# Kernel tuning notes

Hardware: AMD Instinct MI355X
Metric: run time of the kernel (lower is better)

Reference implementation:

```python
import jax, jax.numpy as jnp
import numpy as np
import math

B, L, D, H = 4, 1024, 512, 8
TAU = 0.1
LN_EPS = 1e-5


def _attn(xq, xk, xv, wq, bq, wk, bk, wv, bv, wo, bo, energy=None, threshold=None):
    Bq, Lq, Dm = xq.shape
    Dh = Dm // H
    Q = (xq @ wq.T + bq).reshape(Bq, Lq, H, Dh)
    K = (xk @ wk.T + bk).reshape(Bq, -1, H, Dh)
    V = (xv @ wv.T + bv).reshape(Bq, -1, H, Dh)
    sc = jnp.einsum('bqhd,bkhd->bhqk', Q, K) / jnp.sqrt(jnp.float32(Dh))
    if energy is not None:
        # mask keys whose mean |energy| over channels is below threshold
        mask = jnp.abs(energy).mean(-1)[:, None, None, :] > threshold  # (B,1,1,Lk)
        sc = jnp.where(mask, sc, -jnp.inf)
    w = jnp.nan_to_num(jax.nn.softmax(sc, axis=-1))  # nan->0 for fully-masked rows
    o = jnp.einsum('bhqk,bkhd->bqhd', w, V).reshape(Bq, Lq, Dm)
    return o @ wo.T + bo


def _ln(x, w, b):
    m = x.mean(-1, keepdims=True)
    v = x.var(-1, keepdims=True)
    return (x - m) / jnp.sqrt(v + LN_EPS) * w + b


def _mlp(x, w1, b1, w2, b2):
    h = jax.nn.gelu(x @ w1.T + b1, approximate=False)  # torch nn.GELU default = exact
    return h @ w2.T + b2


def setup_inputs():
    key = jax.random.key(0)
    ks = list(jax.random.split(key, 64))

    def nxt():
        return ks.pop(0)

    def w(shape, scale=0.02):
        return jax.random.normal(nxt(), shape, dtype=jnp.float32) * scale

    inp = {
        'LL': jax.random.normal(nxt(), (B, D, L), dtype=jnp.float32),
        'LH': jax.random.normal(nxt(), (B, D, L), dtype=jnp.float32),
        'raw_tau': jnp.float32(math.log(TAU / (1.0 - TAU))),
    }
    for p in ('llA', 'lhA', 'crA'):
        for nm in ('q', 'k', 'v', 'o'):
            inp[f'{p}_w{nm}'] = w((D, D))
            inp[f'{p}_b{nm}'] = jnp.zeros((D,), jnp.float32)
    for p in ('mlp_ll', 'mlp_lh'):
        inp[f'{p}_w1'] = w((4 * D, D))
        inp[f'{p}_b1'] = jnp.zeros((4 * D,), jnp.float32)
        inp[f'{p}_w2'] = w((D, 4 * D))
        inp[f'{p}_b2'] = jnp.zeros((D,), jnp.float32)
    inp['n1_w'] = jnp.ones((D,), jnp.float32)
    inp['n1_b'] = jnp.zeros((D,), jnp.float32)
    inp['n2_w'] = jnp.ones((D,), jnp.float32)
    inp['n2_b'] = jnp.zeros((D,), jnp.float32)
    return inp


def reference(LL, LH, raw_tau,
              llA_wq, llA_bq, llA_wk, llA_bk, llA_wv, llA_bv, llA_wo, llA_bo,
              lhA_wq, lhA_bq, lhA_wk, lhA_bk, lhA_wv, lhA_bv, lhA_wo, lhA_bo,
              crA_wq, crA_bq, crA_wk, crA_bk, crA_wv, crA_bv, crA_wo, crA_bo,
              mlp_ll_w1, mlp_ll_b1, mlp_ll_w2, mlp_ll_b2,
              mlp_lh_w1, mlp_lh_b1, mlp_lh_w2, mlp_lh_b2,
              n1_w, n1_b, n2_w, n2_b):
    tau = jax.nn.sigmoid(raw_tau)
    ll_s = jnp.transpose(LL, (0, 2, 1))  # (B,L,D)
    lh_s = jnp.transpose(LH, (0, 2, 1))
    ll_o = _attn(ll_s, ll_s, ll_s, llA_wq, llA_bq, llA_wk, llA_bk, llA_wv, llA_bv, llA_wo, llA_bo)
    lh_o = _attn(lh_s, lh_s, lh_s, lhA_wq, lhA_bq, lhA_wk, lhA_bk, lhA_wv, lhA_bv, lhA_wo, lhA_bo,
                 energy=lh_s, threshold=tau)
    cr_o = _attn(ll_o, lh_o, lh_o, crA_wq, crA_bq, crA_wk, crA_bk, crA_wv, crA_bv, crA_wo, crA_bo)
    ll_f = _ln(ll_s + ll_o + cr_o, n1_w, n1_b)
    ll_f = _mlp(ll_f, mlp_ll_w1, mlp_ll_b1, mlp_ll_w2, mlp_ll_b2) + ll_f
    lh_f = _ln(lh_s + lh_o, n2_w, n2_b)
    lh_f = _mlp(lh_f, mlp_lh_w1, mlp_lh_b1, mlp_lh_w2, mlp_lh_b2) + lh_f
    return (jnp.transpose(ll_f, (0, 2, 1)), jnp.transpose(lh_f, (0, 2, 1)))
```

## Files before the change

kernel.cpp:

```cpp
#include <hip/hip_runtime.h>
#include <hip/hip_bf16.h>
#include <stdint.h>

typedef unsigned short u16;
typedef __bf16 bf16_t;
typedef bf16_t bf16x8 __attribute__((ext_vector_type(8)));
typedef float f32x4 __attribute__((ext_vector_type(4)));

#define DEV static __device__ __forceinline__

DEV u16 f2b(float f) {
    __hip_bfloat16 h = __float2bfloat16(f);
    return __builtin_bit_cast(u16, h);
}

DEV bf16x8 ld_frag(const u16* p) {
    uint4 u = *reinterpret_cast<const uint4*>(p);
    return __builtin_bit_cast(bf16x8, u);
}

DEV float gelu(float v) {
    float y = 0.79788456080286536f * (v + 0.044715f * v * v * v);
    float e = __expf(-2.f * fabsf(y));
    float th = (1.f - e) / (1.f + e);
    th = copysignf(th, y);
    return 0.5f * v * (1.f + th);
}

DEV void gl_lds16(const u16* g, u16* l) {
    __builtin_amdgcn_global_load_lds(
        (const __attribute__((address_space(1))) void*)(uintptr_t)g,
        (__attribute__((address_space(3))) void*)(unsigned int)(uintptr_t)l,
        16, 0, 0);
}

struct ConvEnt { const float* s; u16* d; int n; };
struct ConvArgs { ConvEnt e[16]; };

__global__ __launch_bounds__(256) void k_conv(ConvArgs a) {
    const ConvEnt en = a.e[blockIdx.y];
    for (int i = (blockIdx.x * 256 + threadIdx.x) * 4; i < en.n; i += 256 * 256 * 4) {
        const float4 f = *reinterpret_cast<const float4*>(en.s + i);
        unsigned r0 = (unsigned)f2b(f.x) | ((unsigned)f2b(f.y) << 16);
        unsigned r1 = (unsigned)f2b(f.z) | ((unsigned)f2b(f.w) << 16);
        uint2 rr; rr.x = r0; rr.y = r1;
        *reinterpret_cast<uint2*>(en.d + i) = rr;
    }
}

struct CpyEnt { const float* s; float* d; };
struct CpyArgs { CpyEnt e[8]; };

__global__ __launch_bounds__(256) void k_cpyf(CpyArgs a) {
    const CpyEnt en = a.e[blockIdx.y];
    int i = blockIdx.x * 256 + threadIdx.x;
    en.d[i] = en.s[i];
}

__global__ __launch_bounds__(256) void k_tin(const float* __restrict__ LL, const float* __restrict__ LH,
                                             float* __restrict__ llf, u16* __restrict__ llb,
                                             float* __restrict__ lhf, u16* __restrict__ lhb) {
    __shared__ float t[32][33];
    int z = blockIdx.z, b = z & 3;
    const float* in = (z < 4) ? LL : LH;
    float* of = (z < 4) ? llf : lhf;
    u16* ob = (z < 4) ? llb : lhb;
    int l0 = blockIdx.x * 32, d0 = blockIdx.y * 32;
    int tx = threadIdx.x, ty = threadIdx.y;
#pragma unroll
    for (int j = 0; j < 4; ++j) {
        int d = d0 + ty + j * 8;
        t[ty + j * 8][tx] = in[((size_t)b * 512 + d) * 1024 + l0 + tx];
    }
    __syncthreads();
#pragma unroll
    for (int j = 0; j < 4; ++j) {
        int l = l0 + ty + j * 8;
        float v = t[tx][ty + j * 8];
        size_t o = ((size_t)b * 1024 + l) * 512 + d0 + tx;
        of[o] = v;
        ob[o] = f2b(v);
    }
}

__global__ __launch_bounds__(256) void k_tout(const float* __restrict__ y0, const float* __restrict__ y1,
                                              float* __restrict__ out) {
    __shared__ float t[32][33];
    int z = blockIdx.z, b = z & 3;
    const float* in = (z < 4) ? y0 : y1;
    float* o = out + ((z < 4) ? 0 : (size_t)4096 * 512);
    int l0 = blockIdx.x * 32, d0 = blockIdx.y * 32;
    int tx = threadIdx.x, ty = threadIdx.y;
#pragma unroll
    for (int j = 0; j < 4; ++j) {
        int l = l0 + ty + j * 8;
        t[ty + j * 8][tx] = in[((size_t)b * 1024 + l) * 512 + d0 + tx];
    }
    __syncthreads();
#pragma unroll
    for (int j = 0; j < 4; ++j) {
        int d = d0 + ty + j * 8;
        o[((size_t)b * 512 + d) * 1024 + l0 + tx] = t[tx][ty + j * 8];
    }
}

__global__ __launch_bounds__(256) void k_mask(const float* __restrict__ lh_s,
                                              const float* __restrict__ raw_tau,
                                              float* __restrict__ kbias) {
    int row = blockIdx.x * 4 + (threadIdx.x >> 6);
    int lane = threadIdx.x & 63;
    const float* p = lh_s + (size_t)row * 512 + lane * 8;
    float s = 0.f;
#pragma unroll
    for (int j = 0; j < 8; ++j) s += fabsf(p[j]);
#pragma unroll
    for (int m = 32; m >= 1; m >>= 1) s += __shfl_xor(s, m, 64);
    float tau = 1.f / (1.f + expf(-raw_tau[0]));
    if (lane == 0) kbias[row] = (s * (1.f / 512.f) > tau) ? 0.f : -3.0e38f;
}

__global__ __launch_bounds__(256) void k_ln(const float* __restrict__ a, const float* __restrict__ b,
                                            const float* __restrict__ c, const float* __restrict__ w,
                                            const float* __restrict__ bi,
                                            float* __restrict__ of, u16* __restrict__ ob) {
    int row = blockIdx.x * 4 + (threadIdx.x >> 6);
    int lane = threadIdx.x & 63;
    size_t base = (size_t)row * 512 + lane * 8;
    float x[8];
#pragma unroll
    for (int j = 0; j < 8; ++j) {
        float v = a[base + j] + b[base + j];
        if (c) v += c[base + j];
        x[j] = v;
    }
    float s = 0.f, s2 = 0.f;
#pragma unroll
    for (int j = 0; j < 8; ++j) { s += x[j]; s2 += x[j] * x[j]; }
#pragma unroll
    for (int m = 32; m >= 1; m >>= 1) { s += __shfl_xor(s, m, 64); s2 += __shfl_xor(s2, m, 64); }
    float mean = s * (1.f / 512.f);
    float var = s2 * (1.f / 512.f) - mean * mean;
    float rs = rsqrtf(var + 1e-5f);
#pragma unroll
    for (int j = 0; j < 8; ++j) {
        float y = (x[j] - mean) * rs * w[lane * 8 + j] + bi[lane * 8 + j];
        of[base + j] = y;
        ob[base + j] = f2b(y);
    }
}

struct GP {
    const u16* A; const u16* W; const float* bias; const float* res;
    float* Cf; u16* Cb; u16* Qp; u16* Kp; u16* Vt;
    int N, K, kB, vB, nwg;
};

template <int BM, int BN, int GELU_ACT, int PACK>
__global__ __launch_bounds__(256) void k_gemm(GP p0, GP p1, int M) {
    constexpr int BK = 64;
    __shared__ alignas(16) u16 Al[2][BM * BK];
    __shared__ alignas(16) u16 Wl[2][BN * BK];
    GP g = (blockIdx.y == 0) ? p0 : p1;
    const int orig = blockIdx.x;
    if (orig >= g.nwg) return;
    int bid;
    {
        const int xcd = orig & 7, lin = orig >> 3;
        const int q = g.nwg >> 3, r = g.nwg & 7;
        bid = (xcd < r ? xcd * (q + 1) : r * (q + 1) + (xcd - r) * q) + lin;
    }
    const int K = g.K, N = g.N;
    const int nny = N / BN;
    const int m0 = (bid / nny) * BM, n0 = (bid % nny) * BN;

    const int t = threadIdx.x, w = t >> 6, l = t & 63;
    constexpr int FM = BM / 32, FN = BN / 32;
    const int wr = w >> 1, wc = w & 1;
    const int lq = l & 15, lg = l >> 4;
    f32x4 acc[FM][FN] = {};

    const int srow = l >> 3, schunk = l & 7;
    auto stage = [&](int kcol, int buf) {
#pragma unroll
        for (int i = 0; i < BM / 32; ++i) {
            const int row = i * 32 + w * 8 + srow;
            gl_lds16(g.A + (size_t)(m0 + row) * K + kcol + ((schunk ^ (row & 7)) * 8),
                     &Al[buf][(i * 32 + w * 8) * BK]);
        }
#pragma unroll
        for (int i = 0; i < BN / 32; ++i) {
            const int row = i * 32 + w * 8 + srow;
            gl_lds16(g.W + (size_t)(n0 + row) * K + kcol + ((schunk ^ (row & 7)) * 8),
                     &Wl[buf][(i * 32 + w * 8) * BK]);
        }
    };

    stage(0, 0);
    const int KT = K / BK;
    for (int kt = 0; kt < KT; ++kt) {
        const int cur = kt & 1;
        __syncthreads();
        if (kt + 1 < KT) stage((kt + 1) * BK, cur ^ 1);
#pragma unroll
        for (int s = 0; s < 2; ++s) {
            bf16x8 af[FM], bw[FN];
#pragma unroll
            for (int i = 0; i < FM; ++i) {
                const int row = wr * (BM / 2) + i * 16 + lq;
                af[i] = ld_frag(&Al[cur][row * BK + (((s * 4 + lg) ^ (row & 7)) * 8)]);
            }
#pragma unroll
            for (int j = 0; j < FN; ++j) {
                const int row = wc * (BN / 2) + j * 16 + lq;
                bw[j] = ld_frag(&Wl[cur][row * BK + (((s * 4 + lg) ^ (row & 7)) * 8)]);
            }
#pragma unroll
            for (int i = 0; i < FM; ++i)
#pragma unroll
                for (int j = 0; j < FN; ++j)
                    acc[i][j] = __builtin_amdgcn_mfma_f32_16x16x32_bf16(af[i], bw[j], acc[i][j], 0, 0, 0);
        }
    }

    if (PACK && n0 >= g.vB) {
        u16* T = (u16*)Al;
        constexpr int CH = BM / 8, CMASK = CH - 1, SH = (CH == 16) ? 4 : 3;
        __syncthreads();
#pragma unroll
        for (int i = 0; i < FM; ++i) {
#pragma unroll
            for (int j = 0; j < FN; ++j) {
                const int ni = wc * (BN / 2) + j * 16 + lq;
                const float bn = g.bias[n0 + ni];
#pragma unroll
                for (int r2 = 0; r2 < 4; ++r2) {
                    const int mi = wr * (BM / 2) + i * 16 + lg * 4 + r2;
                    T[ni * BM + (((mi >> 3) ^ (ni & CMASK)) * 8) + (mi & 7)] = f2b(acc[i][j][r2] + bn);
                }
            }
        }
        __syncthreads();
        const int bb = m0 >> 10, mloc = m0 & 1023;
        const int mc = t & CMASK, nib = t >> SH;
        constexpr int RPP = 256 / CH;
#pragma unroll
        for (int p2 = 0; p2 < BN / RPP; ++p2) {
            const int ni = nib + p2 * RPP;
            uint4 u = *reinterpret_cast<const uint4*>(&T[ni * BM + ((mc ^ (ni & CMASK)) * 8)]);
            const int d = n0 - g.vB + ni;
            *reinterpret_cast<uint4*>(
                &g.Vt[((size_t)(bb * 8 + (d >> 6)) * 64 + (d & 63)) * 1024 + mloc + mc * 8]) = u;
        }
        return;
    }

#pragma unroll
    for (int i = 0; i < FM; ++i) {
#pragma unroll
        for (int j = 0; j < FN; ++j) {
            const int n = n0 + wc * (BN / 2) + j * 16 + lq;
            const float bn = g.bias[n];
#pragma unroll
            for (int r2 = 0; r2 < 4; ++r2) {
                const int m = m0 + wr * (BM / 2) + i * 16 + lg * 4 + r2;
                float v = acc[i][j][r2] + bn;
                if (GELU_ACT) v = gelu(v);
                if (PACK) {
                    const int bb = m >> 10, ll_ = m & 1023;
                    if (n >= g.kB) {
                        const int d = n - g.kB;
                        g.Kp[((size_t)(bb * 8 + (d >> 6)) * 1024 + ll_) * 64 + (d & 63)] = f2b(v);
                    } else {
                        g.Qp[((size_t)(bb * 8 + (n >> 6)) * 1024 + ll_) * 64 + (n & 63)] = f2b(v * 0.125f);
                    }
                } else {
                    size_t o = (size_t)m * N + n;
                    if (g.res) v += g.res[o];
                    if (g.Cf) g.Cf[o] = v;
                    if (g.Cb) g.Cb[o] = f2b(v);
                }
            }
        }
    }
}

__global__ __launch_bounds__(256) void k_attn(const u16* __restrict__ Qp, const u16* __restrict__ Kp,
                                              const u16* __restrict__ Vtp, u16* __restrict__ O,
                                              const float* __restrict__ kbias, int nwg) {
    constexpr int L = 1024;
    __shared__ alignas(16) u16 Kl[2][64 * 64];
    __shared__ alignas(16) u16 Vl[2][64 * 64];
    __shared__ alignas(16) u16 Pl[128 * 64];
    const int t = threadIdx.x, w = t >> 6, l = t & 63;
    const int bid = ((int)blockIdx.x & 7) * (nwg >> 3) + ((int)blockIdx.x >> 3);
    const int bh = bid >> 3, q0 = (bid & 7) * 128;
    const int bz = bh >> 3, h = bh & 7;
    const int lq = l & 15, lg = l >> 4;
    const float* kb = (kbias != nullptr && bz >= 4) ? (kbias + (size_t)(bz - 4) * L) : nullptr;

    bf16x8 qa[2][2];
#pragma unroll
    for (int i = 0; i < 2; ++i) {
        const u16* qp = Qp + ((size_t)bh * L + q0 + w * 32 + i * 16 + lq) * 64 + lg * 8;
        qa[i][0] = ld_frag(qp);
        qa[i][1] = ld_frag(qp + 32);
    }

    const int r0 = w * 16 + (l >> 3), r1 = r0 + 8, c = l & 7;
    const u16* Ksrc0 = Kp + (size_t)bh * L * 64 + (size_t)r0 * 64 + ((c ^ (r0 & 7)) * 8);
    const u16* Ksrc1 = Kp + (size_t)bh * L * 64 + (size_t)r1 * 64 + ((c ^ (r1 & 7)) * 8);
    const u16* Vsrc0 = Vtp + (size_t)bh * 64 * L + (size_t)r0 * L + ((c ^ (r0 & 7)) * 8);
    const u16* Vsrc1 = Vtp + (size_t)bh * 64 * L + (size_t)r1 * L + ((c ^ (r1 & 7)) * 8);

    auto stage = [&](int k0, int buf) {
        gl_lds16(Ksrc0 + (size_t)k0 * 64, &Kl[buf][(w * 16) * 64]);
        gl_lds16(Ksrc1 + (size_t)k0 * 64, &Kl[buf][(w * 16 + 8) * 64]);
        gl_lds16(Vsrc0 + k0, &Vl[buf][(w * 16) * 64]);
        gl_lds16(Vsrc1 + k0, &Vl[buf][(w * 16 + 8) * 64]);
    };

    int addrA[4][2];
#pragma unroll
    for (int f = 0; f < 4; ++f) {
        int row = f * 16 + lq;
#pragma unroll
        for (int s = 0; s < 2; ++s) addrA[f][s] = row * 64 + (((s * 4 + lg) ^ (row & 7)) * 8);
    }
    int paddr[2][2], pwbase[2];
#pragma unroll
    for (int i = 0; i < 2; ++i) {
        const int prow = w * 32 + i * 16 + lq;
#pragma unroll
        for (int s = 0; s < 2; ++s) paddr[i][s] = prow * 64 + (((s * 4 + lg) ^ (prow & 7)) * 8);
        pwbase[i] = w * 32 + i * 16 + lg * 4;
    }

    f32x4 oacc[2][4] = {};
    float lrow[2][4] = {};

    stage(0, 0);
    for (int kt = 0; kt < 16; ++kt) {
        const int cur = kt & 1;
        __syncthreads();
        if (kt + 1 < 16) stage((kt + 1) * 64, cur ^ 1);

        f32x4 sc[2][4];
#pragma unroll
        for (int f = 0; f < 4; ++f) {
            bf16x8 k0 = ld_frag(&Kl[cur][addrA[f][0]]);
            bf16x8 k1 = ld_frag(&Kl[cur][addrA[f][1]]);
#pragma unroll
            for (int i = 0; i < 2; ++i) {
                f32x4 a = {};
                a = __builtin_amdgcn_mfma_f32_16x16x32_bf16(qa[i][0], k0, a, 0, 0, 0);
                a = __builtin_amdgcn_mfma_f32_16x16x32_bf16(qa[i][1], k1, a, 0, 0, 0);
                sc[i][f] = a;
            }
        }
#pragma unroll
        for (int f = 0; f < 4; ++f) {
            float bv = kb ? kb[kt * 64 + f * 16 + lq] : 0.f;
#pragma unroll
            for (int i = 0; i < 2; ++i) {
#pragma unroll
                for (int r = 0; r < 4; ++r) {
                    float pv = __expf(sc[i][f][r] + bv);
                    lrow[i][r] += pv;
                    const int prow = pwbase[i] + r;
                    Pl[prow * 64 + (((f * 2 + (lq >> 3)) ^ (prow & 7)) * 8) + (lq & 7)] = f2b(pv);
                }
            }
        }
        bf16x8 pa[2][2];
#pragma unroll
        for (int i = 0; i < 2; ++i) {
            pa[i][0] = ld_frag(&Pl[paddr[i][0]]);
            pa[i][1] = ld_frag(&Pl[paddr[i][1]]);
        }
#pragma unroll
        for (int db = 0; db < 4; ++db) {
            bf16x8 v0 = ld_frag(&Vl[cur][addrA[db][0]]);
            bf16x8 v1 = ld_frag(&Vl[cur][addrA[db][1]]);
#pragma unroll
            for (int i = 0; i < 2; ++i) {
                oacc[i][db] = __builtin_amdgcn_mfma_f32_16x16x32_bf16(pa[i][0], v0, oacc[i][db], 0, 0, 0);
                oacc[i][db] = __builtin_amdgcn_mfma_f32_16x16x32_bf16(pa[i][1], v1, oacc[i][db], 0, 0, 0);
            }
        }
    }
#pragma unroll
    for (int i = 0; i < 2; ++i)
#pragma unroll
        for (int r = 0; r < 4; ++r) {
            float v = lrow[i][r];
#pragma unroll
            for (int msk = 8; msk >= 1; msk >>= 1) v += __shfl_xor(v, msk, 16);
            lrow[i][r] = v;
        }
#pragma unroll
    for (int i = 0; i < 2; ++i) {
#pragma unroll
        for (int db = 0; db < 4; ++db) {
#pragma unroll
            for (int r = 0; r < 4; ++r) {
                float denom = lrow[i][r];
                float v = (denom > 0.f) ? oacc[i][db][r] / denom : 0.f;
                O[((size_t)bz * L + q0 + w * 32 + i * 16 + lg * 4 + r) * 512 + h * 64 + db * 16 + lq] = f2b(v);
            }
        }
    }
}

extern "C" void kernel_launch(void* const* d_in, const int* in_sizes, int n_in,
                              void* d_out, int out_size, void* d_ws, size_t ws_size,
                              hipStream_t stream) {
    const int M = 4096;
    const float* LL = (const float*)d_in[0];
    const float* LH = (const float*)d_in[1];
    const float* raw_tau = (const float*)d_in[2];
    auto F = [&](int i) { return (const float*)d_in[i]; };
    const int BIG = 1 << 28;

    char* p = (char*)d_ws;
    auto alloc = [&](size_t bytes) { void* r = (void*)p; p += (bytes + 255) & ~(size_t)255; return r; };
    const size_t MDf = (size_t)M * 512 * 4, MDb = (size_t)M * 512 * 2;
    float* ll_s_f = (float*)alloc(MDf);
    float* lh_s_f = (float*)alloc(MDf);
    u16* ll_s_b = (u16*)alloc(MDb);
    u16* lh_s_b = (u16*)alloc(MDb);
    u16* Qp = (u16*)alloc(2 * MDb);
    u16* Kp = (u16*)alloc(2 * MDb);
    u16* Vt = (u16*)alloc(2 * MDb);
    u16* Cxb = (u16*)alloc(2 * MDb);
    float* ll_o_f = (float*)alloc(MDf);
    u16* ll_o_b = (u16*)alloc(MDb);
    float* lh_o_f = (float*)alloc(MDf);
    u16* lh_o_b = (u16*)alloc(MDb);
    float* cr_o_f = (float*)alloc(MDf);
    float* ln_f_ll = (float*)alloc(MDf);
    float* ln_f_lh = (float*)alloc(MDf);
    u16* ln_b = (u16*)alloc(MDb);
    u16* hb = (u16*)alloc((size_t)M * 2048 * 2);
    float* yf_ll = (float*)alloc(MDf);
    float* yf_lh = (float*)alloc(MDf);
    float* kbias = (float*)alloc(4096 * 4);
    float* bqkv_ll = (float*)alloc(1536 * 4);
    float* bqkv_lh = (float*)alloc(1536 * 4);
    float* bkv_cr = (float*)alloc(1024 * 4);
    const size_t WDD = (size_t)262144;
    u16* wqkv_ll = (u16*)alloc(3 * WDD * 2);
    u16* wqkv_lh = (u16*)alloc(3 * WDD * 2);
    u16* wkv_cr = (u16*)alloc(2 * WDD * 2);
    u16* wq_cr = (u16*)alloc(WDD * 2);
    u16* wo_ll = (u16*)alloc(WDD * 2);
    u16* wo_lh = (u16*)alloc(WDD * 2);
    u16* wo_cr = (u16*)alloc(WDD * 2);
    u16* wm[4];
    for (int i = 0; i < 4; ++i) wm[i] = (u16*)alloc((size_t)1048576 * 2);

    const size_t SET = (size_t)4 * 8 * 1024 * 64;

    ConvArgs ca;
    ca.e[0] = {F(3), wqkv_ll, (int)WDD};
    ca.e[1] = {F(5), wqkv_ll + WDD, (int)WDD};
    ca.e[2] = {F(7), wqkv_ll + 2 * WDD, (int)WDD};
    ca.e[3] = {F(11), wqkv_lh, (int)WDD};
    ca.e[4] = {F(13), wqkv_lh + WDD, (int)WDD};
    ca.e[5] = {F(15), wqkv_lh + 2 * WDD, (int)WDD};
    ca.e[6] = {F(19), wq_cr, (int)WDD};
    ca.e[7] = {F(21), wkv_cr, (int)WDD};
    ca.e[8] = {F(23), wkv_cr + WDD, (int)WDD};
    ca.e[9] = {F(9), wo_ll, (int)WDD};
    ca.e[10] = {F(17), wo_lh, (int)WDD};
    ca.e[11] = {F(25), wo_cr, (int)WDD};
    ca.e[12] = {F(27), wm[0], 1048576};
    ca.e[13] = {F(29), wm[1], 1048576};
    ca.e[14] = {F(31), wm[2], 1048576};
    ca.e[15] = {F(33), wm[3], 1048576};
    k_conv<<<dim3(256, 16), 256, 0, stream>>>(ca);

    CpyArgs cp;
    cp.e[0] = {F(4), bqkv_ll};
    cp.e[1] = {F(6), bqkv_ll + 512};
    cp.e[2] = {F(8), bqkv_ll + 1024};
    cp.e[3] = {F(12), bqkv_lh};
    cp.e[4] = {F(14), bqkv_lh + 512};
    cp.e[5] = {F(16), bqkv_lh + 1024};
    cp.e[6] = {F(22), bkv_cr};
    cp.e[7] = {F(24), bkv_cr + 512};
    k_cpyf<<<dim3(2, 8), 256, 0, stream>>>(cp);

    k_tin<<<dim3(32, 16, 8), dim3(32, 8), 0, stream>>>(LL, LH, ll_s_f, ll_s_b, lh_s_f, lh_s_b);
    k_mask<<<dim3(1024), 256, 0, stream>>>(lh_s_f, raw_tau, kbias);

    auto gp = [&](const u16* A, const u16* W, const float* bias, int N, int K, int nwg) {
        GP g = {};
        g.A = A; g.W = W; g.bias = bias; g.N = N; g.K = K; g.nwg = nwg;
        g.kB = BIG; g.vB = BIG;
        return g;
    };

    {
        GP a = gp(ll_s_b, wqkv_ll, bqkv_ll, 1536, 512, 384);
        a.kB = 512; a.vB = 1024; a.Qp = Qp; a.Kp = Kp; a.Vt = Vt;
        GP b = gp(lh_s_b, wqkv_lh, bqkv_lh, 1536, 512, 384);
        b.kB = 512; b.vB = 1024; b.Qp = Qp + SET; b.Kp = Kp + SET; b.Vt = Vt + SET;
        k_gemm<128, 128, 0, 1><<<dim3(384, 2), 256, 0, stream>>>(a, b, M);
    }
    k_attn<<<dim3(512), 256, 0, stream>>>(Qp, Kp, Vt, Cxb, kbias, 512);
    {
        GP a = gp(Cxb, wo_ll, F(10), 512, 512, 512);
        a.Cf = ll_o_f; a.Cb = ll_o_b;
        GP b = gp(Cxb + SET, wo_lh, F(18), 512, 512, 512);
        b.Cf = lh_o_f; b.Cb = lh_o_b;
        k_gemm<64, 64, 0, 0><<<dim3(512, 2), 256, 0, stream>>>(a, b, M);
    }
    k_ln<<<dim3(1024), 256, 0, stream>>>(lh_s_f, lh_o_f, nullptr, F(37), F(38), ln_f_lh, ln_b);
    {
        GP a = gp(ln_b, wm[2], F(32), 2048, 512, 512);
        a.Cb = hb;
        k_gemm<128, 128, 1, 0><<<dim3(512, 1), 256, 0, stream>>>(a, a, M);
    }
    {
        GP a = gp(ll_o_b, wq_cr, F(20), 512, 512, 512);
        a.Qp = Qp;
        GP b = gp(lh_o_b, wkv_cr, bkv_cr, 1024, 512, 1024);
        b.kB = 0; b.vB = 512; b.Kp = Kp; b.Vt = Vt;
        k_gemm<64, 64, 0, 1><<<dim3(1024, 2), 256, 0, stream>>>(a, b, M);
    }
    k_attn<<<dim3(256), 256, 0, stream>>>(Qp, Kp, Vt, Cxb, nullptr, 256);
    {
        GP a = gp(Cxb, wo_cr, F(26), 512, 512, 512);
        a.Cf = cr_o_f;
        GP b = gp(hb, wm[3], F(34), 512, 2048, 512);
        b.Cf = yf_lh; b.res = ln_f_lh;
        k_gemm<64, 64, 0, 0><<<dim3(512, 2), 256, 0, stream>>>(a, b, M);
    }
    k_ln<<<dim3(1024), 256, 0, stream>>>(ll_s_f, ll_o_f, cr_o_f, F(35), F(36), ln_f_ll, ln_b);
    {
        GP a = gp(ln_b, wm[0], F(28), 2048, 512, 512);
        a.Cb = hb;
        k_gemm<128, 128, 1, 0><<<dim3(512, 1), 256, 0, stream>>>(a, a, M);
    }
    {
        GP a = gp(hb, wm[1], F(30), 512, 2048, 512);
        a.Cf = yf_ll; a.res = ln_f_ll;
        k_gemm<64, 64, 0, 0><<<dim3(512, 1), 256, 0, stream>>>(a, a, M);
    }
    k_tout<<<dim3(32, 16, 8), dim3(32, 8), 0, stream>>>(yf_ll, yf_lh, (float*)d_out);
}
```

Baseline: 268.7 us.

## Fuse attention and independent GEMMs into shared launches to overlap work

Splits the GEMM and attention kernels into device bodies, then adds a combined kernel whose first blocks run attention and whose remaining blocks run an independent GEMM. The LL and LH branches and the cross-attention stages are rescheduled so that attention for one branch overlaps with projection or MLP GEMMs of another, which cuts launch count and fills idle CUs during the low-occupancy attention launches. The Q scale changes to fold in log2(e) so softmax can use exp2f, and the mask bias becomes -inf. This adds shared-memory sizing constraints and load imbalance risk between the mixed block types.

```diff
diff --git a/kernel.cpp b/kernel.cpp
--- a/kernel.cpp
+++ b/kernel.cpp
@@ -8,6 +8,8 @@
 typedef float f32x4 __attribute__((ext_vector_type(4)));
 
 #define DEV static __device__ __forceinline__
+
+#define QSCALE 0.18033688011112042f
 
 DEV u16 f2b(float f) {
     __hip_bfloat16 h = __float2bfloat16(f);
@@ -116,7 +118,7 @@
 #pragma unroll
     for (int m = 32; m >= 1; m >>= 1) s += __shfl_xor(s, m, 64);
     float tau = 1.f / (1.f + expf(-raw_tau[0]));
-    if (lane == 0) kbias[row] = (s * (1.f / 512.f) > tau) ? 0.f : -3.0e38f;
+    if (lane == 0) kbias[row] = (s * (1.f / 512.f) > tau) ? 0.f : -__builtin_inff();
 }
 
 __global__ __launch_bounds__(256) void k_ln(const float* __restrict__ a, const float* __restrict__ b,
@@ -152,17 +154,14 @@
 struct GP {
     const u16* A; const u16* W; const float* bias; const float* res;
     float* Cf; u16* Cb; u16* Qp; u16* Kp; u16* Vt;
-    int N, K, kB, vB, nwg;
+    int N, K, kB, vB, nwg, pack;
 };
 
 template <int BM, int BN, int GELU_ACT, int PACK>
-__global__ __launch_bounds__(256) void k_gemm(GP p0, GP p1, int M) {
+DEV void gemm_body(u16* smem, const GP g, int orig, int M) {
     constexpr int BK = 64;
-    __shared__ alignas(16) u16 Al[2][BM * BK];
-    __shared__ alignas(16) u16 Wl[2][BN * BK];
-    GP g = (blockIdx.y == 0) ? p0 : p1;
-    const int orig = blockIdx.x;
-    if (orig >= g.nwg) return;
+    u16* Al = smem;
+    u16* Wl = smem + 2 * BM * BK;
     int bid;
     {
         const int xcd = orig & 7, lin = orig >> 3;
@@ -185,13 +184,13 @@
         for (int i = 0; i < BM / 32; ++i) {
             const int row = i * 32 + w * 8 + srow;
             gl_lds16(g.A + (size_t)(m0 + row) * K + kcol + ((schunk ^ (row & 7)) * 8),
-                     &Al[buf][(i * 32 + w * 8) * BK]);
+                     &Al[buf * BM * BK + (i * 32 + w * 8) * BK]);
         }
 #pragma unroll
         for (int i = 0; i < BN / 32; ++i) {
             const int row = i * 32 + w * 8 + srow;
             gl_lds16(g.W + (size_t)(n0 + row) * K + kcol + ((schunk ^ (row & 7)) * 8),
-                     &Wl[buf][(i * 32 + w * 8) * BK]);
+                     &Wl[buf * BN * BK + (i * 32 + w * 8) * BK]);
         }
     };
 
@@ -207,12 +206,12 @@
 #pragma unroll
             for (int i = 0; i < FM; ++i) {
                 const int row = wr * (BM / 2) + i * 16 + lq;
-                af[i] = ld_frag(&Al[cur][row * BK + (((s * 4 + lg) ^ (row & 7)) * 8)]);
+                af[i] = ld_frag(&Al[cur * BM * BK + row * BK + (((s * 4 + lg) ^ (row & 7)) * 8)]);
             }
 #pragma unroll
             for (int j = 0; j < FN; ++j) {
                 const int row = wc * (BN / 2) + j * 16 + lq;
-                bw[j] = ld_frag(&Wl[cur][row * BK + (((s * 4 + lg) ^ (row & 7)) * 8)]);
+                bw[j] = ld_frag(&Wl[cur * BN * BK + row * BK + (((s * 4 + lg) ^ (row & 7)) * 8)]);
             }
 #pragma unroll
             for (int i = 0; i < FM; ++i)
@@ -222,8 +221,8 @@
         }
     }
 
-    if (PACK && n0 >= g.vB) {
-        u16* T = (u16*)Al;
+    if (PACK && g.pack && n0 >= g.vB) {
+        u16* T = Al;
         constexpr int CH = BM / 8, CMASK = CH - 1, SH = (CH == 16) ? 4 : 3;
         __syncthreads();
 #pragma unroll
@@ -265,13 +264,13 @@
                 const int m = m0 + wr * (BM / 2) + i * 16 + lg * 4 + r2;
                 float v = acc[i][j][r2] + bn;
                 if (GELU_ACT) v = gelu(v);
-                if (PACK) {
+                if (PACK && g.pack) {
                     const int bb = m >> 10, ll_ = m & 1023;
                     if (n >= g.kB) {
                         const int d = n - g.kB;
                         g.Kp[((size_t)(bb * 8 + (d >> 6)) * 1024 + ll_) * 64 + (d & 63)] = f2b(v);
                     } else {
-                        g.Qp[((size_t)(bb * 8 + (n >> 6)) * 1024 + ll_) * 64 + (n & 63)] = f2b(v * 0.125f);
+                        g.Qp[((size_t)(bb * 8 + (n >> 6)) * 1024 + ll_) * 64 + (n & 63)] = f2b(v * QSCALE);
                     }
                 } else {
                     size_t o = (size_t)m * N + n;
@@ -284,39 +283,47 @@
     }
 }
 
-__global__ __launch_bounds__(256) void k_attn(const u16* __restrict__ Qp, const u16* __restrict__ Kp,
-                                              const u16* __restrict__ Vtp, u16* __restrict__ O,
-                                              const float* __restrict__ kbias, int nwg) {
+template <int BM, int BN, int GELU_ACT, int PACK>
+__global__ __launch_bounds__(256) void k_gemm(GP p0, GP p1, int M) {
+    __shared__ alignas(16) u16 smem[2 * (BM + BN) * 64];
+    GP g = (blockIdx.y == 0) ? p0 : p1;
+    if ((int)blockIdx.x >= g.nwg) return;
+    gemm_body<BM, BN, GELU_ACT, PACK>(smem, g, blockIdx.x, M);
+}
+
+struct AT { const u16* Qp; const u16* Kp; const u16* Vt; u16* O; const float* kbias; };
+
+DEV void attn_body(u16* smem, const AT a, int orig, int nwg) {
     constexpr int L = 1024;
-    __shared__ alignas(16) u16 Kl[2][64 * 64];
-    __shared__ alignas(16) u16 Vl[2][64 * 64];
-    __shared__ alignas(16) u16 Pl[128 * 64];
+    u16* Pl = smem + 16384;
     const int t = threadIdx.x, w = t >> 6, l = t & 63;
-    const int bid = ((int)blockIdx.x & 7) * (nwg >> 3) + ((int)blockIdx.x >> 3);
+    const int bid = (orig & 7) * (nwg >> 3) + (orig >> 3);
     const int bh = bid >> 3, q0 = (bid & 7) * 128;
     const int bz = bh >> 3, h = bh & 7;
     const int lq = l & 15, lg = l >> 4;
-    const float* kb = (kbias != nullptr && bz >= 4) ? (kbias + (size_t)(bz - 4) * L) : nullptr;
+    const float* kb = a.kbias ? (a.kbias + (size_t)bz * L) : nullptr;
 
     bf16x8 qa[2][2];
 #pragma unroll
     for (int i = 0; i < 2; ++i) {
-        const u16* qp = Qp + ((size_t)bh * L + q0 + w * 32 + i * 16 + lq) * 64 + lg * 8;
+        const u16* qp = a.Qp + ((size_t)bh * L + q0 + w * 32 + i * 16 + lq) * 64 + lg * 8;
         qa[i][0] = ld_frag(qp);
         qa[i][1] = ld_frag(qp + 32);
     }
 
     const int r0 = w * 16 + (l >> 3), r1 = r0 + 8, c = l & 7;
-    const u16* Ksrc0 = Kp + (size_t)bh * L * 64 + (size_t)r0 * 64 + ((c ^ (r0 & 7)) * 8);
-    const u16* Ksrc1 = Kp + (size_t)bh * L * 64 + (size_t)r1 * 64 + ((c ^ (r1 & 7)) * 8);
-    const u16* Vsrc0 = Vtp + (size_t)bh * 64 * L + (size_t)r0 * L + ((c ^ (r0 & 7)) * 8);
-    const u16* Vsrc1 = Vtp + (size_t)bh * 64 * L + (size_t)r1 * L + ((c ^ (r1 & 7)) * 8);
+    const u16* Ksrc0 = a.Kp + (size_t)bh * L * 64 + (size_t)r0 * 64 + ((c ^ (r0 & 7)) * 8);
+    const u16* Ksrc1 = a.Kp + (size_t)bh * L * 64 + (size_t)r1 * 64 + ((c ^ (r1 & 7)) * 8);
+    const u16* Vsrc0 = a.Vt + (size_t)bh * 64 * L + (size_t)r0 * L + ((c ^ (r0 & 7)) * 8);
+    const u16* Vsrc1 = a.Vt + (size_t)bh * 64 * L + (size_t)r1 * L + ((c ^ (r1 & 7)) * 8);
 
     auto stage = [&](int k0, int buf) {
-        gl_lds16(Ksrc0 + (size_t)k0 * 64, &Kl[buf][(w * 16) * 64]);
-        gl_lds16(Ksrc1 + (size_t)k0 * 64, &Kl[buf][(w * 16 + 8) * 64]);
-        gl_lds16(Vsrc0 + k0, &Vl[buf][(w * 16) * 64]);
-        gl_lds16(Vsrc1 + k0, &Vl[buf][(w * 16 + 8) * 64]);
+        u16* Kb = smem + buf * 4096;
+        u16* Vb = smem + 8192 + buf * 4096;
+        gl_lds16(Ksrc0 + (size_t)k0 * 64, &Kb[(w * 16) * 64]);
+        gl_lds16(Ksrc1 + (size_t)k0 * 64, &Kb[(w * 16 + 8) * 64]);
+        gl_lds16(Vsrc0 + k0, &Vb[(w * 16) * 64]);
+        gl_lds16(Vsrc1 + k0, &Vb[(w * 16 + 8) * 64]);
     };
 
     int addrA[4][2];
@@ -341,20 +348,22 @@
     stage(0, 0);
     for (int kt = 0; kt < 16; ++kt) {
         const int cur = kt & 1;
+        u16* Kc = smem + cur * 4096;
+        u16* Vc = smem + 8192 + cur * 4096;
         __syncthreads();
         if (kt + 1 < 16) stage((kt + 1) * 64, cur ^ 1);
 
         f32x4 sc[2][4];
 #pragma unroll
         for (int f = 0; f < 4; ++f) {
-            bf16x8 k0 = ld_frag(&Kl[cur][addrA[f][0]]);
-            bf16x8 k1 = ld_frag(&Kl[cur][addrA[f][1]]);
+            bf16x8 k0 = ld_frag(&Kc[addrA[f][0]]);
+            bf16x8 k1 = ld_frag(&Kc[addrA[f][1]]);
 #pragma unroll
             for (int i = 0; i < 2; ++i) {
-                f32x4 a = {};
-                a = __builtin_amdgcn_mfma_f32_16x16x32_bf16(qa[i][0], k0, a, 0, 0, 0);
-                a = __builtin_amdgcn_mfma_f32_16x16x32_bf16(qa[i][1], k1, a, 0, 0, 0);
-                sc[i][f] = a;
+                f32x4 acc = {};
+                acc = __builtin_amdgcn_mfma_f32_16x16x32_bf16(qa[i][0], k0, acc, 0, 0, 0);
+                acc = __builtin_amdgcn_mfma_f32_16x16x32_bf16(qa[i][1], k1, acc, 0, 0, 0);
+                sc[i][f] = acc;
             }
         }
 #pragma unroll
@@ -364,7 +373,7 @@
             for (int i = 0; i < 2; ++i) {
 #pragma unroll
                 for (int r = 0; r < 4; ++r) {
-                    float pv = __expf(sc[i][f][r] + bv);
+                    float pv = exp2f(sc[i][f][r] + bv);
                     lrow[i][r] += pv;
                     const int prow = pwbase[i] + r;
                     Pl[prow * 64 + (((f * 2 + (lq >> 3)) ^ (prow & 7)) * 8) + (lq & 7)] = f2b(pv);
@@ -379,8 +388,8 @@
         }
 #pragma unroll
         for (int db = 0; db < 4; ++db) {
-            bf16x8 v0 = ld_frag(&Vl[cur][addrA[db][0]]);
-            bf16x8 v1 = ld_frag(&Vl[cur][addrA[db][1]]);
+            bf16x8 v0 = ld_frag(&Vc[addrA[db][0]]);
+            bf16x8 v1 = ld_frag(&Vc[addrA[db][1]]);
 #pragma unroll
             for (int i = 0; i < 2; ++i) {
                 oacc[i][db] = __builtin_amdgcn_mfma_f32_16x16x32_bf16(pa[i][0], v0, oacc[i][db], 0, 0, 0);
@@ -405,10 +414,21 @@
             for (int r = 0; r < 4; ++r) {
                 float denom = lrow[i][r];
                 float v = (denom > 0.f) ? oacc[i][db][r] / denom : 0.f;
-                O[((size_t)bz * L + q0 + w * 32 + i * 16 + lg * 4 + r) * 512 + h * 64 + db * 16 + lq] = f2b(v);
-            }
-        }
-    }
+                a.O[((size_t)bz * L + q0 + w * 32 + i * 16 + lg * 4 + r) * 512 + h * 64 + db * 16 + lq] = f2b(v);
+            }
+        }
+    }
+}
+
+template <int BM, int BN, int GELU_ACT, int PACK>
+__global__ __launch_bounds__(256) void k_fattn(AT a, GP g, int nAttn, int M) {
+    constexpr int GS = 2 * (BM + BN) * 64;
+    constexpr int SZ = (GS > 24576) ? GS : 24576;
+    __shared__ alignas(16) u16 smem[SZ];
+    if ((int)blockIdx.x < nAttn)
+        attn_body(smem, a, blockIdx.x, nAttn);
+    else
+        gemm_body<BM, BN, GELU_ACT, PACK>(smem, g, blockIdx.x - nAttn, M);
 }
 
 extern "C" void kernel_launch(void* const* d_in, const int* in_sizes, int n_in,
@@ -496,39 +516,46 @@
     auto gp = [&](const u16* A, const u16* W, const float* bias, int N, int K, int nwg) {
         GP g = {};
         g.A = A; g.W = W; g.bias = bias; g.N = N; g.K = K; g.nwg = nwg;
-        g.kB = BIG; g.vB = BIG;
+        g.kB = BIG; g.vB = BIG; g.pack = 0;
         return g;
     };
 
     {
         GP a = gp(ll_s_b, wqkv_ll, bqkv_ll, 1536, 512, 384);
-        a.kB = 512; a.vB = 1024; a.Qp = Qp; a.Kp = Kp; a.Vt = Vt;
-        GP b = gp(lh_s_b, wqkv_lh, bqkv_lh, 1536, 512, 384);
-        b.kB = 512; b.vB = 1024; b.Qp = Qp + SET; b.Kp = Kp + SET; b.Vt = Vt + SET;
-        k_gemm<128, 128, 0, 1><<<dim3(384, 2), 256, 0, stream>>>(a, b, M);
-    }
-    k_attn<<<dim3(512), 256, 0, stream>>>(Qp, Kp, Vt, Cxb, kbias, 512);
-    {
-        GP a = gp(Cxb, wo_ll, F(10), 512, 512, 512);
-        a.Cf = ll_o_f; a.Cb = ll_o_b;
-        GP b = gp(Cxb + SET, wo_lh, F(18), 512, 512, 512);
-        b.Cf = lh_o_f; b.Cb = lh_o_b;
-        k_gemm<64, 64, 0, 0><<<dim3(512, 2), 256, 0, stream>>>(a, b, M);
+        a.pack = 1; a.kB = 512; a.vB = 1024; a.Qp = Qp; a.Kp = Kp; a.Vt = Vt;
+        k_gemm<128, 128, 0, 1><<<dim3(384, 1), 256, 0, stream>>>(a, a, M);
+    }
+    {
+        AT at = {Qp, Kp, Vt, Cxb, nullptr};
+        GP g = gp(lh_s_b, wqkv_lh, bqkv_lh, 1536, 512, 384);
+        g.pack = 1; g.kB = 512; g.vB = 1024; g.Qp = Qp + SET; g.Kp = Kp + SET; g.Vt = Vt + SET;
+        k_fattn<128, 128, 0, 1><<<dim3(640), 256, 0, stream>>>(at, g, 256, M);
+    }
+    {
+        AT at = {Qp + SET, Kp + SET, Vt + SET, Cxb + SET, kbias};
+        GP g = gp(Cxb, wo_ll, F(10), 512, 512, 512);
+        g.Cf = ll_o_f; g.Cb = ll_o_b;
+        k_fattn<64, 64, 0, 1><<<dim3(768), 256, 0, stream>>>(at, g, 256, M);
+    }
+    {
+        GP a = gp(Cxb + SET, wo_lh, F(18), 512, 512, 512);
+        a.Cf = lh_o_f; a.Cb = lh_o_b;
+        GP b = gp(ll_o_b, wq_cr, F(20), 512, 512, 512);
+        b.pack = 1; b.Qp = Qp;
+        k_gemm<64, 64, 0, 1><<<dim3(512, 2), 256, 0, stream>>>(a, b, M);
     }
     k_ln<<<dim3(1024), 256, 0, stream>>>(lh_s_f, lh_o_f, nullptr, F(37), F(38), ln_f_lh, ln_b);
     {
-        GP a = gp(ln_b, wm[2], F(32), 2048, 512, 512);
-        a.Cb = hb;
-        k_gemm<128, 128, 1, 0><<<dim3(512, 1), 256, 0, stream>>>(a, a, M);
-    }
-    {
-        GP a = gp(ll_o_b, wq_cr, F(20), 512, 512, 512);
-        a.Qp = Qp;
-        GP b = gp(lh_o_b, wkv_cr, bkv_cr, 1024, 512, 1024);
-        b.kB = 0; b.vB = 512; b.Kp = Kp; b.Vt = Vt;
-        k_gemm<64, 64, 0, 1><<<dim3(1024, 2), 256, 0, stream>>>(a, b, M);
-    }
-    k_attn<<<dim3(256), 256, 0, stream>>>(Qp, Kp, Vt, Cxb, nullptr, 256);
+        GP a = gp(lh_o_b, wkv_cr, bkv_cr, 1024, 512, 1024);
+        a.pack = 1; a.kB = 0; a.vB = 512; a.Kp = Kp; a.Vt = Vt;
+        k_gemm<64, 64, 0, 1><<<dim3(1024, 1), 256, 0, stream>>>(a, a, M);
+    }
+    {
+        AT at = {Qp, Kp, Vt, Cxb, nullptr};
+        GP g = gp(ln_b, wm[2], F(32), 2048, 512, 512);
+        g.Cb = hb;
+        k_fattn<128, 128, 1, 0><<<dim3(768), 256, 0, stream>>>(at, g, 256, M);
+    }
     {
         GP a = gp(Cxb, wo_cr, F(26), 512, 512, 512);
         a.Cf = cr_o_f;
```

New measurement: 298.1 us. 10.9% more time.

## Split attention over key halves with separate combine kernel, use exp2 and setprio

Applied to the files above, without the earlier changes.

Attention work is split along the key dimension into two halves per query tile, doubling the number of workgroups. Each half writes unnormalized fp32 numerators and row sums to scratch, and a new combine kernel adds the halves and normalizes. Q is now prescaled by log2(e)/8 so exp2f can replace __expf, the mask bias becomes -inf, and s_setprio is raised around the MFMA sections. This adds a scratch round trip and an extra launch in exchange for higher occupancy. There is no running-max subtraction, so overflow behaviour depends on the score magnitudes.

```diff
diff --git a/kernel.cpp b/kernel.cpp
--- a/kernel.cpp
+++ b/kernel.cpp
@@ -8,6 +8,8 @@
 typedef float f32x4 __attribute__((ext_vector_type(4)));
 
 #define DEV static __device__ __forceinline__
+
+#define QSCALE 0.18033688011112042f
 
 DEV u16 f2b(float f) {
     __hip_bfloat16 h = __float2bfloat16(f);
@@ -116,7 +118,7 @@
 #pragma unroll
     for (int m = 32; m >= 1; m >>= 1) s += __shfl_xor(s, m, 64);
     float tau = 1.f / (1.f + expf(-raw_tau[0]));
-    if (lane == 0) kbias[row] = (s * (1.f / 512.f) > tau) ? 0.f : -3.0e38f;
+    if (lane == 0) kbias[row] = (s * (1.f / 512.f) > tau) ? 0.f : -__builtin_inff();
 }
 
 __global__ __launch_bounds__(256) void k_ln(const float* __restrict__ a, const float* __restrict__ b,
@@ -271,7 +273,7 @@
                         const int d = n - g.kB;
                         g.Kp[((size_t)(bb * 8 + (d >> 6)) * 1024 + ll_) * 64 + (d & 63)] = f2b(v);
                     } else {
-                        g.Qp[((size_t)(bb * 8 + (n >> 6)) * 1024 + ll_) * 64 + (n & 63)] = f2b(v * 0.125f);
+                        g.Qp[((size_t)(bb * 8 + (n >> 6)) * 1024 + ll_) * 64 + (n & 63)] = f2b(v * QSCALE);
                     }
                 } else {
                     size_t o = (size_t)m * N + n;
@@ -284,19 +286,23 @@
     }
 }
 
-__global__ __launch_bounds__(256) void k_attn(const u16* __restrict__ Qp, const u16* __restrict__ Kp,
-                                              const u16* __restrict__ Vtp, u16* __restrict__ O,
-                                              const float* __restrict__ kbias, int nwg) {
+__global__ __launch_bounds__(256) void k_attnK(const u16* __restrict__ Qp, const u16* __restrict__ Kp,
+                                               const u16* __restrict__ Vtp,
+                                               float* __restrict__ numW, float* __restrict__ denW,
+                                               const float* __restrict__ kbias, int nwg) {
     constexpr int L = 1024;
     __shared__ alignas(16) u16 Kl[2][64 * 64];
     __shared__ alignas(16) u16 Vl[2][64 * 64];
     __shared__ alignas(16) u16 Pl[128 * 64];
     const int t = threadIdx.x, w = t >> 6, l = t & 63;
     const int bid = ((int)blockIdx.x & 7) * (nwg >> 3) + ((int)blockIdx.x >> 3);
-    const int bh = bid >> 3, q0 = (bid & 7) * 128;
+    const int item = bid >> 1, half = bid & 1;
+    const int bh = item >> 3, q0 = (item & 7) * 128;
     const int bz = bh >> 3, h = bh & 7;
+    (void)h;
     const int lq = l & 15, lg = l >> 4;
     const float* kb = (kbias != nullptr && bz >= 4) ? (kbias + (size_t)(bz - 4) * L) : nullptr;
+    const int kbase = half * 512;
 
     bf16x8 qa[2][2];
 #pragma unroll
@@ -338,13 +344,14 @@
     f32x4 oacc[2][4] = {};
     float lrow[2][4] = {};
 
-    stage(0, 0);
-    for (int kt = 0; kt < 16; ++kt) {
+    stage(kbase, 0);
+    for (int kt = 0; kt < 8; ++kt) {
         const int cur = kt & 1;
         __syncthreads();
-        if (kt + 1 < 16) stage((kt + 1) * 64, cur ^ 1);
+        if (kt + 1 < 8) stage(kbase + (kt + 1) * 64, cur ^ 1);
 
         f32x4 sc[2][4];
+        __builtin_amdgcn_s_setprio(1);
 #pragma unroll
         for (int f = 0; f < 4; ++f) {
             bf16x8 k0 = ld_frag(&Kl[cur][addrA[f][0]]);
@@ -357,14 +364,15 @@
                 sc[i][f] = a;
             }
         }
+        __builtin_amdgcn_s_setprio(0);
 #pragma unroll
         for (int f = 0; f < 4; ++f) {
-            float bv = kb ? kb[kt * 64 + f * 16 + lq] : 0.f;
+            float bv = kb ? kb[kbase + kt * 64 + f * 16 + lq] : 0.f;
 #pragma unroll
             for (int i = 0; i < 2; ++i) {
 #pragma unroll
                 for (int r = 0; r < 4; ++r) {
-                    float pv = __expf(sc[i][f][r] + bv);
+                    float pv = exp2f(sc[i][f][r] + bv);
                     lrow[i][r] += pv;
                     const int prow = pwbase[i] + r;
                     Pl[prow * 64 + (((f * 2 + (lq >> 3)) ^ (prow & 7)) * 8) + (lq & 7)] = f2b(pv);
@@ -377,6 +385,7 @@
             pa[i][0] = ld_frag(&Pl[paddr[i][0]]);
             pa[i][1] = ld_frag(&Pl[paddr[i][1]]);
         }
+        __builtin_amdgcn_s_setprio(1);
 #pragma unroll
         for (int db = 0; db < 4; ++db) {
             bf16x8 v0 = ld_frag(&Vl[cur][addrA[db][0]]);
@@ -387,6 +396,7 @@
                 oacc[i][db] = __builtin_amdgcn_mfma_f32_16x16x32_bf16(pa[i][1], v1, oacc[i][db], 0, 0, 0);
             }
         }
+        __builtin_amdgcn_s_setprio(0);
     }
 #pragma unroll
     for (int i = 0; i < 2; ++i)
@@ -397,17 +407,49 @@
             for (int msk = 8; msk >= 1; msk >>= 1) v += __shfl_xor(v, msk, 16);
             lrow[i][r] = v;
         }
+    float* nw = numW + (size_t)bid * 8192;
 #pragma unroll
     for (int i = 0; i < 2; ++i) {
 #pragma unroll
         for (int db = 0; db < 4; ++db) {
 #pragma unroll
             for (int r = 0; r < 4; ++r) {
-                float denom = lrow[i][r];
-                float v = (denom > 0.f) ? oacc[i][db][r] / denom : 0.f;
-                O[((size_t)bz * L + q0 + w * 32 + i * 16 + lg * 4 + r) * 512 + h * 64 + db * 16 + lq] = f2b(v);
-            }
-        }
+                nw[(pwbase[i] + r) * 64 + db * 16 + lq] = oacc[i][db][r];
+            }
+        }
+    }
+    if (lq == 0) {
+#pragma unroll
+        for (int i = 0; i < 2; ++i)
+#pragma unroll
+            for (int r = 0; r < 4; ++r) denW[(size_t)bid * 128 + pwbase[i] + r] = lrow[i][r];
+    }
+}
+
+__global__ __launch_bounds__(256) void k_comb(const float* __restrict__ numW,
+                                              const float* __restrict__ denW,
+                                              u16* __restrict__ O) {
+    const int item = blockIdx.x, t = threadIdx.x;
+    const int bh = item >> 3, q0 = (item & 7) * 128;
+    const int bz = bh >> 3, h = bh & 7;
+    const float4* n0 = (const float4*)(numW + (size_t)(item * 2) * 8192);
+    const float4* n1 = (const float4*)(numW + (size_t)(item * 2 + 1) * 8192);
+    const float* d0 = denW + (size_t)(item * 2) * 128;
+    const float* d1 = denW + (size_t)(item * 2 + 1) * 128;
+#pragma unroll
+    for (int e = 0; e < 8; ++e) {
+        const int g = e * 256 + t;
+        const int row = g >> 4, c4 = (g & 15) * 4;
+        float4 a = n0[g], b = n1[g];
+        float den = d0[row] + d1[row];
+        float inv = (den > 0.f) ? 1.f / den : 0.f;
+        u16 o4[4];
+        o4[0] = f2b((a.x + b.x) * inv);
+        o4[1] = f2b((a.y + b.y) * inv);
+        o4[2] = f2b((a.z + b.z) * inv);
+        o4[3] = f2b((a.w + b.w) * inv);
+        *reinterpret_cast<uint2*>(&O[((size_t)bz * 1024 + q0 + row) * 512 + h * 64 + c4]) =
+            *reinterpret_cast<uint2*>(o4);
     }
 }
 
@@ -447,6 +489,8 @@
     float* bqkv_ll = (float*)alloc(1536 * 4);
     float* bqkv_lh = (float*)alloc(1536 * 4);
     float* bkv_cr = (float*)alloc(1024 * 4);
+    float* numW = (float*)alloc((size_t)1024 * 8192 * 4);
+    float* denW = (float*)alloc((size_t)1024 * 128 * 4);
     const size_t WDD = (size_t)262144;
     u16* wqkv_ll = (u16*)alloc(3 * WDD * 2);
     u16* wqkv_lh = (u16*)alloc(3 * WDD * 2);
@@ -507,7 +551,8 @@
         b.kB = 512; b.vB = 1024; b.Qp = Qp + SET; b.Kp = Kp + SET; b.Vt = Vt + SET;
         k_gemm<128, 128, 0, 1><<<dim3(384, 2), 256, 0, stream>>>(a, b, M);
     }
-    k_attn<<<dim3(512), 256, 0, stream>>>(Qp, Kp, Vt, Cxb, kbias, 512);
+    k_attnK<<<dim3(1024), 256, 0, stream>>>(Qp, Kp, Vt, numW, denW, kbias, 1024);
+    k_comb<<<dim3(512), 256, 0, stream>>>(numW, denW, Cxb);
     {
         GP a = gp(Cxb, wo_ll, F(10), 512, 512, 512);
         a.Cf = ll_o_f; a.Cb = ll_o_b;
@@ -528,7 +573,8 @@
         b.kB = 0; b.vB = 512; b.Kp = Kp; b.Vt = Vt;
         k_gemm<64, 64, 0, 1><<<dim3(1024, 2), 256, 0, stream>>>(a, b, M);
     }
-    k_attn<<<dim3(256), 256, 0, stream>>>(Qp, Kp, Vt, Cxb, nullptr, 256);
+    k_attnK<<<dim3(512), 256, 0, stream>>>(Qp, Kp, Vt, numW, denW, nullptr, 512);
+    k_comb<<<dim3(256), 256, 0, stream>>>(numW, denW, Cxb);
     {
         GP a = gp(Cxb, wo_cr, F(26), 512, 512, 512);
         a.Cf = cr_o_f;
```

After: 285.7 us. +6.3%, slower.

## Load attention K/V fragments directly from global into registers and use exp2

Applied to the files above, without the earlier changes.

The attention kernel stops staging K and V tiles through double-buffered LDS with block-wide barriers. Each wave now reads its MFMA fragments straight from global memory into registers and prefetches the next K tile while the current one is in use. The softmax uses exp2 by folding log2(e) into the Q pre-scale, wraps the MFMA sections in s_setprio, and uses -inf as the mask bias. This removes LDS traffic and __syncthreads, but every wave now fetches K/V itself, which adds redundant global/L2 reads across the four waves.

```diff
diff --git a/kernel.cpp b/kernel.cpp
--- a/kernel.cpp
+++ b/kernel.cpp
@@ -8,6 +8,8 @@
 typedef float f32x4 __attribute__((ext_vector_type(4)));
 
 #define DEV static __device__ __forceinline__
+
+#define QSCALE 0.18033688011112042f
 
 DEV u16 f2b(float f) {
     __hip_bfloat16 h = __float2bfloat16(f);
@@ -116,7 +118,7 @@
 #pragma unroll
     for (int m = 32; m >= 1; m >>= 1) s += __shfl_xor(s, m, 64);
     float tau = 1.f / (1.f + expf(-raw_tau[0]));
-    if (lane == 0) kbias[row] = (s * (1.f / 512.f) > tau) ? 0.f : -3.0e38f;
+    if (lane == 0) kbias[row] = (s * (1.f / 512.f) > tau) ? 0.f : -__builtin_inff();
 }
 
 __global__ __launch_bounds__(256) void k_ln(const float* __restrict__ a, const float* __restrict__ b,
@@ -271,7 +273,7 @@
                         const int d = n - g.kB;
                         g.Kp[((size_t)(bb * 8 + (d >> 6)) * 1024 + ll_) * 64 + (d & 63)] = f2b(v);
                     } else {
-                        g.Qp[((size_t)(bb * 8 + (n >> 6)) * 1024 + ll_) * 64 + (n & 63)] = f2b(v * 0.125f);
+                        g.Qp[((size_t)(bb * 8 + (n >> 6)) * 1024 + ll_) * 64 + (n & 63)] = f2b(v * QSCALE);
                     }
                 } else {
                     size_t o = (size_t)m * N + n;
@@ -288,8 +290,6 @@
                                               const u16* __restrict__ Vtp, u16* __restrict__ O,
                                               const float* __restrict__ kbias, int nwg) {
     constexpr int L = 1024;
-    __shared__ alignas(16) u16 Kl[2][64 * 64];
-    __shared__ alignas(16) u16 Vl[2][64 * 64];
     __shared__ alignas(16) u16 Pl[128 * 64];
     const int t = threadIdx.x, w = t >> 6, l = t & 63;
     const int bid = ((int)blockIdx.x & 7) * (nwg >> 3) + ((int)blockIdx.x >> 3);
@@ -306,26 +306,9 @@
         qa[i][1] = ld_frag(qp + 32);
     }
 
-    const int r0 = w * 16 + (l >> 3), r1 = r0 + 8, c = l & 7;
-    const u16* Ksrc0 = Kp + (size_t)bh * L * 64 + (size_t)r0 * 64 + ((c ^ (r0 & 7)) * 8);
-    const u16* Ksrc1 = Kp + (size_t)bh * L * 64 + (size_t)r1 * 64 + ((c ^ (r1 & 7)) * 8);
-    const u16* Vsrc0 = Vtp + (size_t)bh * 64 * L + (size_t)r0 * L + ((c ^ (r0 & 7)) * 8);
-    const u16* Vsrc1 = Vtp + (size_t)bh * 64 * L + (size_t)r1 * L + ((c ^ (r1 & 7)) * 8);
-
-    auto stage = [&](int k0, int buf) {
-        gl_lds16(Ksrc0 + (size_t)k0 * 64, &Kl[buf][(w * 16) * 64]);
-        gl_lds16(Ksrc1 + (size_t)k0 * 64, &Kl[buf][(w * 16 + 8) * 64]);
-        gl_lds16(Vsrc0 + k0, &Vl[buf][(w * 16) * 64]);
-        gl_lds16(Vsrc1 + k0, &Vl[buf][(w * 16 + 8) * 64]);
-    };
-
-    int addrA[4][2];
-#pragma unroll
-    for (int f = 0; f < 4; ++f) {
-        int row = f * 16 + lq;
-#pragma unroll
-        for (int s = 0; s < 2; ++s) addrA[f][s] = row * 64 + (((s * 4 + lg) ^ (row & 7)) * 8);
-    }
+    const u16* Kbase = Kp + (size_t)bh * L * 64 + (size_t)lq * 64 + lg * 8;
+    const u16* Vbase = Vtp + (size_t)bh * 64 * L + (size_t)lq * L + lg * 8;
+
     int paddr[2][2], pwbase[2];
 #pragma unroll
     for (int i = 0; i < 2; ++i) {
@@ -338,24 +321,43 @@
     f32x4 oacc[2][4] = {};
     float lrow[2][4] = {};
 
-    stage(0, 0);
+    bf16x8 kf[4][2];
+#pragma unroll
+    for (int f = 0; f < 4; ++f)
+#pragma unroll
+        for (int s = 0; s < 2; ++s)
+            kf[f][s] = ld_frag(Kbase + f * 1024 + s * 32);
+
     for (int kt = 0; kt < 16; ++kt) {
-        const int cur = kt & 1;
-        __syncthreads();
-        if (kt + 1 < 16) stage((kt + 1) * 64, cur ^ 1);
-
         f32x4 sc[2][4];
+        __builtin_amdgcn_s_setprio(1);
 #pragma unroll
         for (int f = 0; f < 4; ++f) {
-            bf16x8 k0 = ld_frag(&Kl[cur][addrA[f][0]]);
-            bf16x8 k1 = ld_frag(&Kl[cur][addrA[f][1]]);
 #pragma unroll
             for (int i = 0; i < 2; ++i) {
                 f32x4 a = {};
-                a = __builtin_amdgcn_mfma_f32_16x16x32_bf16(qa[i][0], k0, a, 0, 0, 0);
-                a = __builtin_amdgcn_mfma_f32_16x16x32_bf16(qa[i][1], k1, a, 0, 0, 0);
+                a = __builtin_amdgcn_mfma_f32_16x16x32_bf16(qa[i][0], kf[f][0], a, 0, 0, 0);
+                a = __builtin_amdgcn_mfma_f32_16x16x32_bf16(qa[i][1], kf[f][1], a, 0, 0, 0);
                 sc[i][f] = a;
             }
+        }
+        __builtin_amdgcn_s_setprio(0);
+        if (kt + 1 < 16) {
+            const u16* kp = Kbase + (kt + 1) * 4096;
+#pragma unroll
+            for (int f = 0; f < 4; ++f)
+#pragma unroll
+                for (int s = 0; s < 2; ++s)
+                    kf[f][s] = ld_frag(kp + f * 1024 + s * 32);
+        }
+        bf16x8 vf[4][2];
+        {
+            const u16* vp = Vbase + kt * 64;
+#pragma unroll
+            for (int db = 0; db < 4; ++db)
+#pragma unroll
+                for (int s = 0; s < 2; ++s)
+                    vf[db][s] = ld_frag(vp + (size_t)db * 16 * L + s * 32);
         }
 #pragma unroll
         for (int f = 0; f < 4; ++f) {
@@ -364,7 +366,7 @@
             for (int i = 0; i < 2; ++i) {
 #pragma unroll
                 for (int r = 0; r < 4; ++r) {
-                    float pv = __expf(sc[i][f][r] + bv);
+                    float pv = exp2f(sc[i][f][r] + bv);
                     lrow[i][r] += pv;
                     const int prow = pwbase[i] + r;
                     Pl[prow * 64 + (((f * 2 + (lq >> 3)) ^ (prow & 7)) * 8) + (lq & 7)] = f2b(pv);
@@ -377,16 +379,16 @@
             pa[i][0] = ld_frag(&Pl[paddr[i][0]]);
             pa[i][1] = ld_frag(&Pl[paddr[i][1]]);
         }
+        __builtin_amdgcn_s_setprio(1);
 #pragma unroll
         for (int db = 0; db < 4; ++db) {
-            bf16x8 v0 = ld_frag(&Vl[cur][addrA[db][0]]);
-            bf16x8 v1 = ld_frag(&Vl[cur][addrA[db][1]]);
 #pragma unroll
             for (int i = 0; i < 2; ++i) {
-                oacc[i][db] = __builtin_amdgcn_mfma_f32_16x16x32_bf16(pa[i][0], v0, oacc[i][db], 0, 0, 0);
-                oacc[i][db] = __builtin_amdgcn_mfma_f32_16x16x32_bf16(pa[i][1], v1, oacc[i][db], 0, 0, 0);
-            }
-        }
+                oacc[i][db] = __builtin_amdgcn_mfma_f32_16x16x32_bf16(pa[i][0], vf[db][0], oacc[i][db], 0, 0, 0);
+                oacc[i][db] = __builtin_amdgcn_mfma_f32_16x16x32_bf16(pa[i][1], vf[db][1], oacc[i][db], 0, 0, 0);
+            }
+        }
+        __builtin_amdgcn_s_setprio(0);
     }
 #pragma unroll
     for (int i = 0; i < 2; ++i)
```

Measured after the change: 352.2 us. +31.1%, slower.
